# Kernel optimization log

Measured on AMD Instinct MI355X. Metric: run time of the kernel, lower is better.

## Reference

```python
import jax, jax.numpy as jnp
import numpy as np
import math

B, S, D, H = 2, 2048, 1024, 16
DK = D // H

def setup_inputs() -> dict:
    key = jax.random.key(0)
    ks = jax.random.split(key, 12)
    def xavier(k, shape):
        fan_in, fan_out = shape[1], shape[0]
        limit = math.sqrt(6.0 / (fan_in + fan_out))
        return jax.random.uniform(k, shape, jnp.float32, -limit, limit)
    inp = {
        'query': jax.random.normal(ks[0], (B, S, D), jnp.float32),
        'key':   jax.random.normal(ks[1], (B, S, D), jnp.float32),
        'value': jax.random.normal(ks[2], (B, S, D), jnp.float32),
        # causal mask, broadcast over heads: (B, 1, S, S), 1 = keep, 0 = mask
        'mask':  jnp.broadcast_to(jnp.tril(jnp.ones((S, S), jnp.int32)), (B, 1, S, S)),
        'Wq': xavier(ks[3], (D, D)), 'bq': jnp.zeros((D,), jnp.float32),
        'Wk': xavier(ks[4], (D, D)), 'bk': jnp.zeros((D,), jnp.float32),
        'Wv': xavier(ks[5], (D, D)), 'bv': jnp.zeros((D,), jnp.float32),
        'Wo': xavier(ks[6], (D, D)), 'bo': jnp.zeros((D,), jnp.float32),
    }
    return inp

def _split_heads(x):
    # (B, S, D) -> (B, H, S, DK)
    b, s, _ = x.shape
    return x.reshape(b, s, H, DK).transpose(0, 2, 1, 3)

def reference(query, key, value, mask, Wq, bq, Wk, bk, Wv, bv, Wo, bo):
    # torch nn.Linear: y = x @ W.T + b
    Q = _split_heads(query @ Wq.T + bq)   # (B,H,S,DK)
    K = _split_heads(key   @ Wk.T + bk)
    V = _split_heads(value @ Wv.T + bv)
    scores = jnp.einsum('bhqd,bhkd->bhqk', Q, K) / math.sqrt(DK)  # (B,H,S,S)
    scores = jnp.where(mask == 0, jnp.float32(-1e9), scores)
    attn = jax.nn.softmax(scores, axis=-1)  # dropout p=0 -> identity
    out = jnp.einsum('bhqk,bhkd->bhqd', attn, V)  # (B,H,S,DK)
    out = out.transpose(0, 2, 1, 3).reshape(query.shape[0], query.shape[1], D)
    return out @ Wo.T + bo
```

## Files before the change

### kernel.cpp

```cpp
#include <hip/hip_runtime.h>
#include <hip/hip_bf16.h>
#include <type_traits>


typedef __attribute__((ext_vector_type(8))) short short8;
typedef __attribute__((ext_vector_type(4))) short s16x4;
typedef __attribute__((ext_vector_type(4))) float floatx4;

__device__ __forceinline__ short f2bf(float x) {
    union { float f; unsigned u; } v; v.f = x;
    unsigned r = v.u + 0x7fffu + ((v.u >> 16) & 1u);
    return (short)(r >> 16);
}

__device__ __forceinline__ unsigned pk2bf(float a, float b) {
    union { __hip_bfloat162 h2; unsigned u; } cv;
    cv.h2 = __float22bfloat162_rn(make_float2(a, b));
    return cv.u;
}

__device__ __forceinline__ float fast_exp2(float x) {
#if __has_builtin(__builtin_amdgcn_exp2f)
    return __builtin_amdgcn_exp2f(x);
#else
    return __expf(x * 0.69314718056f);
#endif
}

typedef __attribute__((address_space(3))) short lds_short;
typedef __attribute__((address_space(1))) const short glb_short;
__device__ __forceinline__ void load_lds16(const void* g, void* l) {
    __builtin_amdgcn_global_load_lds((glb_short*)g, (lds_short*)l, 16, 0, 0);
}

__global__ __launch_bounds__(256) void cvt_all(
        const float* __restrict__ q, const float* __restrict__ k,
        const float* __restrict__ v,
        const float* __restrict__ wq, const float* __restrict__ wk,
        const float* __restrict__ wv, const float* __restrict__ wo,
        unsigned short* __restrict__ xq, unsigned short* __restrict__ xk,
        unsigned short* __restrict__ xv,
        unsigned short* __restrict__ wqb, unsigned short* __restrict__ wkb,
        unsigned short* __restrict__ wvb, unsigned short* __restrict__ wob) {
    const float* s; unsigned short* d;
    int bx = blockIdx.x;
    switch (blockIdx.y) {
        case 0: s = q; d = xq; break;
        case 1: s = k; d = xk; break;
        case 2: s = v; d = xv; break;
        default: {
            int wsel = bx >> 9; bx &= 511;
            s = (wsel == 0) ? wq : (wsel == 1) ? wk : (wsel == 2) ? wv : wo;
            d = (wsel == 0) ? wqb : (wsel == 1) ? wkb : (wsel == 2) ? wvb : wob;
        }
    }
    size_t i = ((size_t)bx * 256 + threadIdx.x) * 8;
    floatx4 a = *(const floatx4*)(s + i), b2 = *(const floatx4*)(s + i + 4);
    union { unsigned u[4]; short8 v8; } o;
    o.u[0] = pk2bf(a[0], a[1]);  o.u[1] = pk2bf(a[2], a[3]);
    o.u[2] = pk2bf(b2[0], b2[1]); o.u[3] = pk2bf(b2[2], b2[3]);
    *(short8*)(d + i) = o.v8;
}

__global__ __launch_bounds__(256) void gemm_qkv(
        const unsigned short* __restrict__ Xq, const unsigned short* __restrict__ Xk,
        const unsigned short* __restrict__ Xv,
        const unsigned short* __restrict__ Wq, const unsigned short* __restrict__ Wk,
        const unsigned short* __restrict__ Wv,
        const float* __restrict__ bq, const float* __restrict__ bk,
        const float* __restrict__ bv,
        unsigned short* __restrict__ Qb, unsigned short* __restrict__ Kb,
        unsigned short* __restrict__ Vb) {
    constexpr int K = 1024, N = 1024;
    __shared__ short As[128 * 64];
    __shared__ short Bs[128 * 64];
    const int t = threadIdx.x;
    const int slot = blockIdx.x;
    const int p = (slot & 7) + 8 * (slot >> 6);
    const int nx = (slot >> 3) & 7;
    const int chunk = p >> 5, my = p & 31;
    const unsigned short* A = chunk == 0 ? Xq : chunk == 1 ? Xk : Xv;
    const unsigned short* W = chunk == 0 ? Wq : chunk == 1 ? Wk : Wv;
    const float* bias        = chunk == 0 ? bq : chunk == 1 ? bk : bv;
    unsigned short* Y        = chunk == 0 ? Qb : chunk == 1 ? Kb : Vb;
    const float scale = chunk == 0 ? 0.1803368801f : 1.0f;
    const int m0 = my * 128, n0 = nx * 128;
    const int lane = t & 63, w = t >> 6;
    const int l16 = lane & 15, quad = lane >> 4;
    const int wm = w >> 1, wn = w & 1;
    const int srow8 = t >> 3, scs8 = t & 7;
    floatx4 acc[4][4] = {};

    for (int k0 = 0; k0 < K; k0 += 64) {
        __syncthreads();
        for (int i = 0; i < 4; i++) {
            const int row = i * 32 + srow8;
            const int cg = scs8 ^ (row & 7);
            load_lds16(A + (size_t)(m0 + row) * K + k0 + cg * 8, &As[i * 2048 + t * 8]);
            load_lds16(W + (size_t)(n0 + row) * K + k0 + cg * 8, &Bs[i * 2048 + t * 8]);
        }
        __syncthreads();

        for (int kc = 0; kc < 2; kc++) {
            short8 af[4], bf[4];
            for (int ms = 0; ms < 4; ms++) {
                const int row = wm * 64 + ms * 16 + l16;
                af[ms] = *(short8*)&As[row * 64 + (((kc << 2) | quad) ^ (row & 7)) * 8];
            }
            for (int ns = 0; ns < 4; ns++) {
                const int row = wn * 64 + ns * 16 + l16;
                bf[ns] = *(short8*)&Bs[row * 64 + (((kc << 2) | quad) ^ (row & 7)) * 8];
            }
            for (int ms = 0; ms < 4; ms++)
                for (int ns = 0; ns < 4; ns++)
                    acc[ms][ns] = __builtin_amdgcn_mfma_f32_16x16x32_bf16(
                            af[ms], bf[ns], acc[ms][ns], 0, 0, 0);
        }
    }

    for (int ms = 0; ms < 4; ms++)
        for (int ns = 0; ns < 4; ns++) {
            int col = n0 + wn * 64 + ns * 16 + l16;
            float bb = bias[col];
            for (int r = 0; r < 4; r++) {
                int row = m0 + wm * 64 + ms * 16 + quad * 4 + r;
                Y[(size_t)row * N + col] =
                    (unsigned short)f2bf((acc[ms][ns][r] + bb) * scale);
            }
        }
}

__global__ __launch_bounds__(256) void gemm_o(
        const unsigned short* __restrict__ A, const unsigned short* __restrict__ W,
        const float* __restrict__ bo, float* __restrict__ out) {
    constexpr int K = 1024, N = 1024;
    __shared__ short As[128 * 64];
    __shared__ short Bs[64 * 64];
    const int t = threadIdx.x;
    const int slot = blockIdx.x;
    const int z = slot >> 6;
    const int pm = (slot & 7) + 8 * (z >> 1);
    const int nx = ((slot >> 3) & 7) + 8 * (z & 1);
    const int m0 = pm * 128, n0 = nx * 64;
    const int lane = t & 63, w = t >> 6;
    const int l16 = lane & 15, quad = lane >> 4;
    const int wm = w >> 1, wn = w & 1;
    const int srow8 = t >> 3, scs8 = t & 7;
    floatx4 acc[4][2] = {};

    for (int k0 = 0; k0 < K; k0 += 64) {
        __syncthreads();
        for (int i = 0; i < 4; i++) {
            const int row = i * 32 + srow8;
            const int cg = scs8 ^ (row & 7);
            load_lds16(A + (size_t)(m0 + row) * K + k0 + cg * 8, &As[i * 2048 + t * 8]);
        }
        for (int i = 0; i < 2; i++) {
            const int row = i * 32 + srow8;
            const int cg = scs8 ^ (row & 7);
            load_lds16(W + (size_t)(n0 + row) * K + k0 + cg * 8, &Bs[i * 2048 + t * 8]);
        }
        __syncthreads();

        for (int kc = 0; kc < 2; kc++) {
            short8 af[4], bf[2];
            for (int ms = 0; ms < 4; ms++) {
                const int row = wm * 64 + ms * 16 + l16;
                af[ms] = *(short8*)&As[row * 64 + (((kc << 2) | quad) ^ (row & 7)) * 8];
            }
            for (int ns = 0; ns < 2; ns++) {
                const int row = wn * 32 + ns * 16 + l16;
                bf[ns] = *(short8*)&Bs[row * 64 + (((kc << 2) | quad) ^ (row & 7)) * 8];
            }
            for (int ms = 0; ms < 4; ms++)
                for (int ns = 0; ns < 2; ns++)
                    acc[ms][ns] = __builtin_amdgcn_mfma_f32_16x16x32_bf16(
                            af[ms], bf[ns], acc[ms][ns], 0, 0, 0);
        }
    }

    for (int ms = 0; ms < 4; ms++)
        for (int ns = 0; ns < 2; ns++) {
            int col = n0 + wn * 32 + ns * 16 + l16;
            float bb = bo[col];
            for (int r = 0; r < 4; r++) {
                int row = m0 + wm * 64 + ms * 16 + quad * 4 + r;
                out[(size_t)row * N + col] = acc[ms][ns][r] + bb;
            }
        }
}

__global__ __launch_bounds__(256) void attn_kernel(
        const unsigned short* __restrict__ Q, const unsigned short* __restrict__ Kp,
        const unsigned short* __restrict__ Vp, unsigned short* __restrict__ O) {
    __shared__ short Ks[64 * 72];
    __shared__ short Vt[64 * 72];
    __shared__ short Ps[4][16 * 72];
    const int t = threadIdx.x;
    const int bx = blockIdx.x;
    const int g = bx >> 8, c = bx & 255;
    const int dlt = c >> 5, bh = c & 31;
    const int unit = (g == 0) ? 31 - dlt : (g == 1) ? 23 - dlt
                   : (g == 2) ? 8 + dlt  : dlt;
    const int h = bh & 15, b = bh >> 4;
    const int q0 = unit * 64;
    const int lane = t & 63, w = t >> 6, l16 = lane & 15, quad = lane >> 4;
    const int krow = t >> 2, kcg = (t & 3) * 16;
    const int vp2 = t & 31, vg = t >> 5;

    short8 qf[2];
    {
        const size_t base = ((size_t)(b * 2048 + q0 + w * 16 + l16)) * 1024 + h * 64;
        qf[0] = *(const short8*)(Q + base + quad * 8);
        qf[1] = *(const short8*)(Q + base + 32 + quad * 8);
    }
    float l = 0.f;
    floatx4 o[4] = {};

    short8 ka, kb, va, vc;
    {
        const size_t kbse = ((size_t)(b * 2048 + krow)) * 1024 + h * 64 + kcg;
        ka = *(const short8*)(Kp + kbse);
        kb = *(const short8*)(Kp + kbse + 8);
        const size_t vbse = ((size_t)(b * 2048 + 2 * vp2)) * 1024 + h * 64 + vg * 8;
        va = *(const short8*)(Vp + vbse);
        vc = *(const short8*)(Vp + vbse + 1024);
    }

    for (int kv0 = 0; kv0 <= q0; kv0 += 64) {
        __syncthreads();
        *(short8*)&Ks[krow * 72 + kcg] = ka;
        *(short8*)&Ks[krow * 72 + kcg + 8] = kb;
        for (int i = 0; i < 8; i++) {
            unsigned pk = (unsigned)(unsigned short)va[i] |
                          ((unsigned)(unsigned short)vc[i] << 16);
            *(unsigned*)&Vt[(vg * 8 + i) * 72 + 2 * vp2] = pk;
        }
        __syncthreads();

        if (kv0 < q0) {
            const size_t kbse = ((size_t)(b * 2048 + kv0 + 64 + krow)) * 1024 + h * 64 + kcg;
            ka = *(const short8*)(Kp + kbse);
            kb = *(const short8*)(Kp + kbse + 8);
            const size_t vbse = ((size_t)(b * 2048 + kv0 + 64 + 2 * vp2)) * 1024 + h * 64 + vg * 8;
            va = *(const short8*)(Vp + vbse);
            vc = *(const short8*)(Vp + vbse + 1024);
        }

        floatx4 sv[4] = {};
        for (int hh = 0; hh < 4; hh++)
            for (int kc = 0; kc < 2; kc++) {
                short8 kf = *(short8*)&Ks[(hh * 16 + l16) * 72 + kc * 32 + quad * 8];
                sv[hh] = __builtin_amdgcn_mfma_f32_16x16x32_bf16(kf, qf[kc], sv[hh], 0, 0, 0);
            }

        {
            const bool needmask = (kv0 + 63 > q0 + w * 16);
            const int qg = q0 + w * 16 + l16;
            float ls = 0.f;
            for (int hh = 0; hh < 4; hh++) {
                float pv[4];
                for (int r = 0; r < 4; r++) {
                    int kv = kv0 + hh * 16 + quad * 4 + r;
                    float e = fast_exp2(sv[hh][r]);
                    pv[r] = (needmask && kv > qg) ? 0.f : e;
                    ls += pv[r];
                }
                union { unsigned u[2]; s16x4 v4; } pw;
                pw.u[0] = pk2bf(pv[0], pv[1]); pw.u[1] = pk2bf(pv[2], pv[3]);
                *(s16x4*)&Ps[w][l16 * 72 + hh * 16 + quad * 4] = pw.v4;
            }
            ls += __shfl_xor(ls, 16);
            ls += __shfl_xor(ls, 32);
            l += ls;
        }

        short8 p0 = *(short8*)&Ps[w][l16 * 72 + quad * 8];
        short8 p1 = *(short8*)&Ps[w][l16 * 72 + 32 + quad * 8];
        for (int nc = 0; nc < 4; nc++) {
            short8 vf0 = *(short8*)&Vt[(nc * 16 + l16) * 72 + quad * 8];
            short8 vf1 = *(short8*)&Vt[(nc * 16 + l16) * 72 + 32 + quad * 8];
            o[nc] = __builtin_amdgcn_mfma_f32_16x16x32_bf16(vf0, p0, o[nc], 0, 0, 0);
            o[nc] = __builtin_amdgcn_mfma_f32_16x16x32_bf16(vf1, p1, o[nc], 0, 0, 0);
        }
    }

    const float rl = 1.f / l;
    const size_t orow = ((size_t)(b * 2048 + q0 + w * 16 + l16)) * 1024 + h * 64;
    for (int nc = 0; nc < 4; nc++) {
        union { unsigned u[2]; s16x4 v4; } ow;
        ow.u[0] = pk2bf(o[nc][0] * rl, o[nc][1] * rl);
        ow.u[1] = pk2bf(o[nc][2] * rl, o[nc][3] * rl);
        *(s16x4*)(O + orow + nc * 16 + quad * 4) = ow.v4;
    }
}

extern "C" void kernel_launch(void* const* d_in, const int* in_sizes, int n_in,
                              void* d_out, int out_size, void* d_ws, size_t ws_size,
                              hipStream_t stream) {
    const float* query = (const float*)d_in[0];
    const float* key   = (const float*)d_in[1];
    const float* value = (const float*)d_in[2];
    const float* Wq = (const float*)d_in[4];
    const float* bq = (const float*)d_in[5];
    const float* Wk = (const float*)d_in[6];
    const float* bk = (const float*)d_in[7];
    const float* Wv = (const float*)d_in[8];
    const float* bv = (const float*)d_in[9];
    const float* Wo = (const float*)d_in[10];
    const float* bo = (const float*)d_in[11];

    const size_t NE = (size_t)4096 * 1024;
    const size_t WE = (size_t)1024 * 1024;
    unsigned short* Xq  = (unsigned short*)d_ws;
    unsigned short* Xk  = Xq + NE;
    unsigned short* Xv  = Xk + NE;
    unsigned short* Qb  = Xv + NE;
    unsigned short* Kb  = Qb + NE;
    unsigned short* Vb  = Kb + NE;
    unsigned short* Ob  = Vb + NE;
    unsigned short* Wqb = Ob + NE;
    unsigned short* Wkb = Wqb + WE;
    unsigned short* Wvb = Wkb + WE;
    unsigned short* Wob = Wvb + WE;

    cvt_all<<<dim3(2048, 4), 256, 0, stream>>>(query, key, value, Wq, Wk, Wv, Wo,
                                               Xq, Xk, Xv, Wqb, Wkb, Wvb, Wob);
    gemm_qkv<<<dim3(768), 256, 0, stream>>>(Xq, Xk, Xv, Wqb, Wkb, Wvb,
                                            bq, bk, bv, Qb, Kb, Vb);
    attn_kernel<<<dim3(1024), 256, 0, stream>>>(Qb, Kb, Vb, Ob);
    gemm_o<<<dim3(512), 256, 0, stream>>>(Ob, Wob, bo, (float*)d_out);
}
```

Measured before the change: 233.3 us.

## Fuse fp32-to-bf16 activation conversion into QKV GEMM and prioritize attention MFMAs

Drops the separate conversion pass over query/key/value. The QKV GEMM now reads fp32 activations straight into registers, converts them to bf16 and writes them to LDS, prefetching the next K-tile into registers while the current tile is computed. This removes the write and re-read of three bf16 activation copies, at the cost of extra registers and VALU conversion work inside the GEMM. Separately, it raises wave priority around the MFMA sections in the attention kernel so the matrix work is scheduled ahead of other waves.

```diff
diff --git a/kernel.cpp b/kernel.cpp
--- a/kernel.cpp
+++ b/kernel.cpp
@@ -33,27 +33,16 @@
     __builtin_amdgcn_global_load_lds((glb_short*)g, (lds_short*)l, 16, 0, 0);
 }
 
-__global__ __launch_bounds__(256) void cvt_all(
-        const float* __restrict__ q, const float* __restrict__ k,
-        const float* __restrict__ v,
+__global__ __launch_bounds__(256) void cvt_w(
         const float* __restrict__ wq, const float* __restrict__ wk,
         const float* __restrict__ wv, const float* __restrict__ wo,
-        unsigned short* __restrict__ xq, unsigned short* __restrict__ xk,
-        unsigned short* __restrict__ xv,
         unsigned short* __restrict__ wqb, unsigned short* __restrict__ wkb,
         unsigned short* __restrict__ wvb, unsigned short* __restrict__ wob) {
-    const float* s; unsigned short* d;
     int bx = blockIdx.x;
-    switch (blockIdx.y) {
-        case 0: s = q; d = xq; break;
-        case 1: s = k; d = xk; break;
-        case 2: s = v; d = xv; break;
-        default: {
-            int wsel = bx >> 9; bx &= 511;
-            s = (wsel == 0) ? wq : (wsel == 1) ? wk : (wsel == 2) ? wv : wo;
-            d = (wsel == 0) ? wqb : (wsel == 1) ? wkb : (wsel == 2) ? wvb : wob;
-        }
-    }
+    const int wsel = bx >> 9; bx &= 511;
+    const float* s = (wsel == 0) ? wq : (wsel == 1) ? wk : (wsel == 2) ? wv : wo;
+    unsigned short* d = (wsel == 0) ? wqb : (wsel == 1) ? wkb
+                      : (wsel == 2) ? wvb : wob;
     size_t i = ((size_t)bx * 256 + threadIdx.x) * 8;
     floatx4 a = *(const floatx4*)(s + i), b2 = *(const floatx4*)(s + i + 4);
     union { unsigned u[4]; short8 v8; } o;
@@ -63,8 +52,8 @@
 }
 
 __global__ __launch_bounds__(256) void gemm_qkv(
-        const unsigned short* __restrict__ Xq, const unsigned short* __restrict__ Xk,
-        const unsigned short* __restrict__ Xv,
+        const float* __restrict__ Xq, const float* __restrict__ Xk,
+        const float* __restrict__ Xv,
         const unsigned short* __restrict__ Wq, const unsigned short* __restrict__ Wk,
         const unsigned short* __restrict__ Wv,
         const float* __restrict__ bq, const float* __restrict__ bk,
@@ -79,10 +68,10 @@
     const int p = (slot & 7) + 8 * (slot >> 6);
     const int nx = (slot >> 3) & 7;
     const int chunk = p >> 5, my = p & 31;
-    const unsigned short* A = chunk == 0 ? Xq : chunk == 1 ? Xk : Xv;
+    const float* A          = chunk == 0 ? Xq : chunk == 1 ? Xk : Xv;
     const unsigned short* W = chunk == 0 ? Wq : chunk == 1 ? Wk : Wv;
-    const float* bias        = chunk == 0 ? bq : chunk == 1 ? bk : bv;
-    unsigned short* Y        = chunk == 0 ? Qb : chunk == 1 ? Kb : Vb;
+    const float* bias       = chunk == 0 ? bq : chunk == 1 ? bk : bv;
+    unsigned short* Y       = chunk == 0 ? Qb : chunk == 1 ? Kb : Vb;
     const float scale = chunk == 0 ? 0.1803368801f : 1.0f;
     const int m0 = my * 128, n0 = nx * 128;
     const int lane = t & 63, w = t >> 6;
@@ -90,16 +79,43 @@
     const int wm = w >> 1, wn = w & 1;
     const int srow8 = t >> 3, scs8 = t & 7;
     floatx4 acc[4][4] = {};
+    floatx4 ar[8];
+
+#pragma unroll
+    for (int i = 0; i < 4; i++) {
+        const int row = i * 32 + srow8;
+        const int cg = scs8 ^ (row & 7);
+        const float* pa = A + (size_t)(m0 + row) * K + cg * 8;
+        ar[2 * i]     = *(const floatx4*)pa;
+        ar[2 * i + 1] = *(const floatx4*)(pa + 4);
+    }
 
     for (int k0 = 0; k0 < K; k0 += 64) {
         __syncthreads();
+#pragma unroll
         for (int i = 0; i < 4; i++) {
+            union { unsigned u[4]; short8 v8; } oa;
+            oa.u[0] = pk2bf(ar[2 * i][0], ar[2 * i][1]);
+            oa.u[1] = pk2bf(ar[2 * i][2], ar[2 * i][3]);
+            oa.u[2] = pk2bf(ar[2 * i + 1][0], ar[2 * i + 1][1]);
+            oa.u[3] = pk2bf(ar[2 * i + 1][2], ar[2 * i + 1][3]);
+            *(short8*)&As[i * 2048 + t * 8] = oa.v8;
             const int row = i * 32 + srow8;
             const int cg = scs8 ^ (row & 7);
-            load_lds16(A + (size_t)(m0 + row) * K + k0 + cg * 8, &As[i * 2048 + t * 8]);
             load_lds16(W + (size_t)(n0 + row) * K + k0 + cg * 8, &Bs[i * 2048 + t * 8]);
         }
         __syncthreads();
+
+        if (k0 + 64 < K) {
+#pragma unroll
+            for (int i = 0; i < 4; i++) {
+                const int row = i * 32 + srow8;
+                const int cg = scs8 ^ (row & 7);
+                const float* pa = A + (size_t)(m0 + row) * K + k0 + 64 + cg * 8;
+                ar[2 * i]     = *(const floatx4*)pa;
+                ar[2 * i + 1] = *(const floatx4*)(pa + 4);
+            }
+        }
 
         for (int kc = 0; kc < 2; kc++) {
             short8 af[4], bf[4];
@@ -248,11 +264,13 @@
         }
 
         floatx4 sv[4] = {};
+        __builtin_amdgcn_s_setprio(1);
         for (int hh = 0; hh < 4; hh++)
             for (int kc = 0; kc < 2; kc++) {
                 short8 kf = *(short8*)&Ks[(hh * 16 + l16) * 72 + kc * 32 + quad * 8];
                 sv[hh] = __builtin_amdgcn_mfma_f32_16x16x32_bf16(kf, qf[kc], sv[hh], 0, 0, 0);
             }
+        __builtin_amdgcn_s_setprio(0);
 
         {
             const bool needmask = (kv0 + 63 > q0 + w * 16);
@@ -277,12 +295,14 @@
 
         short8 p0 = *(short8*)&Ps[w][l16 * 72 + quad * 8];
         short8 p1 = *(short8*)&Ps[w][l16 * 72 + 32 + quad * 8];
+        __builtin_amdgcn_s_setprio(1);
         for (int nc = 0; nc < 4; nc++) {
             short8 vf0 = *(short8*)&Vt[(nc * 16 + l16) * 72 + quad * 8];
             short8 vf1 = *(short8*)&Vt[(nc * 16 + l16) * 72 + 32 + quad * 8];
             o[nc] = __builtin_amdgcn_mfma_f32_16x16x32_bf16(vf0, p0, o[nc], 0, 0, 0);
             o[nc] = __builtin_amdgcn_mfma_f32_16x16x32_bf16(vf1, p1, o[nc], 0, 0, 0);
         }
+        __builtin_amdgcn_s_setprio(0);
     }
 
     const float rl = 1.f / l;
@@ -312,10 +332,7 @@
 
     const size_t NE = (size_t)4096 * 1024;
     const size_t WE = (size_t)1024 * 1024;
-    unsigned short* Xq  = (unsigned short*)d_ws;
-    unsigned short* Xk  = Xq + NE;
-    unsigned short* Xv  = Xk + NE;
-    unsigned short* Qb  = Xv + NE;
+    unsigned short* Qb  = (unsigned short*)d_ws;
     unsigned short* Kb  = Qb + NE;
     unsigned short* Vb  = Kb + NE;
     unsigned short* Ob  = Vb + NE;
@@ -324,9 +341,8 @@
     unsigned short* Wvb = Wkb + WE;
     unsigned short* Wob = Wvb + WE;
 
-    cvt_all<<<dim3(2048, 4), 256, 0, stream>>>(query, key, value, Wq, Wk, Wv, Wo,
-                                               Xq, Xk, Xv, Wqb, Wkb, Wvb, Wob);
-    gemm_qkv<<<dim3(768), 256, 0, stream>>>(Xq, Xk, Xv, Wqb, Wkb, Wvb,
+    cvt_w<<<dim3(2048), 256, 0, stream>>>(Wq, Wk, Wv, Wo, Wqb, Wkb, Wvb, Wob);
+    gemm_qkv<<<dim3(768), 256, 0, stream>>>(query, key, value, Wqb, Wkb, Wvb,
                                             bq, bk, bv, Qb, Kb, Vb);
     attn_kernel<<<dim3(1024), 256, 0, stream>>>(Qb, Kb, Vb, Ob);
     gemm_o<<<dim3(512), 256, 0, stream>>>(Ob, Wob, bo, (float*)d_out);
```

Measured after the change: 244.7 us. 4.9% more time.

## Double query tile per attention block to reuse K/V tiles across two row groups

Applied to the files above, without the earlier changes.

Each attention block now handles 128 query rows instead of 64, with each wave computing two 16-row groups that share the same K and V tiles in shared memory. This halves the grid to 512 blocks and halves the global K/V loads and LDS staging per query row. It also remaps the block-to-tile schedule for causal load balance and raises wave priority around the MFMA sections. The cost is higher register use from doubled accumulators, fewer blocks to fill the GPU, and extra masked work on the diagonal tiles.

```diff
diff --git a/kernel.cpp b/kernel.cpp
--- a/kernel.cpp
+++ b/kernel.cpp
@@ -195,27 +195,28 @@
         const unsigned short* __restrict__ Vp, unsigned short* __restrict__ O) {
     __shared__ short Ks[64 * 72];
     __shared__ short Vt[64 * 72];
-    __shared__ short Ps[4][16 * 72];
+    __shared__ short Ps[8][16 * 72];
     const int t = threadIdx.x;
     const int bx = blockIdx.x;
-    const int g = bx >> 8, c = bx & 255;
-    const int dlt = c >> 5, bh = c & 31;
-    const int unit = (g == 0) ? 31 - dlt : (g == 1) ? 23 - dlt
-                   : (g == 2) ? 8 + dlt  : dlt;
+    const int g = (bx >> 5) & 15, bh = bx & 31;
+    const int tile = (bx < 256) ? (15 - g) : (g - 8);
     const int h = bh & 15, b = bh >> 4;
-    const int q0 = unit * 64;
+    const int q0 = tile * 128;
     const int lane = t & 63, w = t >> 6, l16 = lane & 15, quad = lane >> 4;
     const int krow = t >> 2, kcg = (t & 3) * 16;
     const int vp2 = t & 31, vg = t >> 5;
 
-    short8 qf[2];
+    short8 qa[2], qb[2];
     {
-        const size_t base = ((size_t)(b * 2048 + q0 + w * 16 + l16)) * 1024 + h * 64;
-        qf[0] = *(const short8*)(Q + base + quad * 8);
-        qf[1] = *(const short8*)(Q + base + 32 + quad * 8);
-    }
-    float l = 0.f;
-    floatx4 o[4] = {};
+        const size_t baseA = ((size_t)(b * 2048 + q0 + w * 32 + l16)) * 1024 + h * 64;
+        qa[0] = *(const short8*)(Q + baseA + quad * 8);
+        qa[1] = *(const short8*)(Q + baseA + 32 + quad * 8);
+        const size_t baseB = baseA + (size_t)16 * 1024;
+        qb[0] = *(const short8*)(Q + baseB + quad * 8);
+        qb[1] = *(const short8*)(Q + baseB + 32 + quad * 8);
+    }
+    float lA = 0.f, lB = 0.f;
+    floatx4 oA[4] = {}, oB[4] = {};
 
     short8 ka, kb, va, vc;
     {
@@ -227,7 +228,8 @@
         vc = *(const short8*)(Vp + vbse + 1024);
     }
 
-    for (int kv0 = 0; kv0 <= q0; kv0 += 64) {
+    const int kv_hi = q0 + 128;
+    for (int kv0 = 0; kv0 < kv_hi; kv0 += 64) {
         __syncthreads();
         *(short8*)&Ks[krow * 72 + kcg] = ka;
         *(short8*)&Ks[krow * 72 + kcg + 8] = kb;
@@ -238,7 +240,7 @@
         }
         __syncthreads();
 
-        if (kv0 < q0) {
+        if (kv0 + 64 < kv_hi) {
             const size_t kbse = ((size_t)(b * 2048 + kv0 + 64 + krow)) * 1024 + h * 64 + kcg;
             ka = *(const short8*)(Kp + kbse);
             kb = *(const short8*)(Kp + kbse + 8);
@@ -247,51 +249,92 @@
             vc = *(const short8*)(Vp + vbse + 1024);
         }
 
-        floatx4 sv[4] = {};
+        floatx4 sA[4] = {}, sB[4] = {};
+        __builtin_amdgcn_s_setprio(1);
         for (int hh = 0; hh < 4; hh++)
             for (int kc = 0; kc < 2; kc++) {
                 short8 kf = *(short8*)&Ks[(hh * 16 + l16) * 72 + kc * 32 + quad * 8];
-                sv[hh] = __builtin_amdgcn_mfma_f32_16x16x32_bf16(kf, qf[kc], sv[hh], 0, 0, 0);
-            }
+                sA[hh] = __builtin_amdgcn_mfma_f32_16x16x32_bf16(kf, qa[kc], sA[hh], 0, 0, 0);
+                sB[hh] = __builtin_amdgcn_mfma_f32_16x16x32_bf16(kf, qb[kc], sB[hh], 0, 0, 0);
+            }
+        __builtin_amdgcn_s_setprio(0);
 
         {
-            const bool needmask = (kv0 + 63 > q0 + w * 16);
-            const int qg = q0 + w * 16 + l16;
+            const bool nm = (kv0 + 63 > q0 + w * 32);
+            const int qg = q0 + w * 32 + l16;
             float ls = 0.f;
             for (int hh = 0; hh < 4; hh++) {
                 float pv[4];
                 for (int r = 0; r < 4; r++) {
                     int kv = kv0 + hh * 16 + quad * 4 + r;
-                    float e = fast_exp2(sv[hh][r]);
-                    pv[r] = (needmask && kv > qg) ? 0.f : e;
+                    float e = fast_exp2(sA[hh][r]);
+                    pv[r] = (nm && kv > qg) ? 0.f : e;
                     ls += pv[r];
                 }
                 union { unsigned u[2]; s16x4 v4; } pw;
                 pw.u[0] = pk2bf(pv[0], pv[1]); pw.u[1] = pk2bf(pv[2], pv[3]);
-                *(s16x4*)&Ps[w][l16 * 72 + hh * 16 + quad * 4] = pw.v4;
+                *(s16x4*)&Ps[2 * w][l16 * 72 + hh * 16 + quad * 4] = pw.v4;
             }
             ls += __shfl_xor(ls, 16);
             ls += __shfl_xor(ls, 32);
-            l += ls;
-        }
-
-        short8 p0 = *(short8*)&Ps[w][l16 * 72 + quad * 8];
-        short8 p1 = *(short8*)&Ps[w][l16 * 72 + 32 + quad * 8];
+            lA += ls;
+        }
+        {
+            const bool nm = (kv0 + 63 > q0 + w * 32 + 16);
+            const int qg = q0 + w * 32 + 16 + l16;
+            float ls = 0.f;
+            for (int hh = 0; hh < 4; hh++) {
+                float pv[4];
+                for (int r = 0; r < 4; r++) {
+                    int kv = kv0 + hh * 16 + quad * 4 + r;
+                    float e = fast_exp2(sB[hh][r]);
+                    pv[r] = (nm && kv > qg) ? 0.f : e;
+                    ls += pv[r];
+                }
+                union { unsigned u[2]; s16x4 v4; } pw;
+                pw.u[0] = pk2bf(pv[0], pv[1]); pw.u[1] = pk2bf(pv[2], pv[3]);
+                *(s16x4*)&Ps[2 * w + 1][l16 * 72 + hh * 16 + quad * 4] = pw.v4;
+            }
+            ls += __shfl_xor(ls, 16);
+            ls += __shfl_xor(ls, 32);
+            lB += ls;
+        }
+
+        short8 pa0 = *(short8*)&Ps[2 * w][l16 * 72 + quad * 8];
+        short8 pa1 = *(short8*)&Ps[2 * w][l16 * 72 + 32 + quad * 8];
+        short8 pb0 = *(short8*)&Ps[2 * w + 1][l16 * 72 + quad * 8];
+        short8 pb1 = *(short8*)&Ps[2 * w + 1][l16 * 72 + 32 + quad * 8];
+        __builtin_amdgcn_s_setprio(1);
         for (int nc = 0; nc < 4; nc++) {
             short8 vf0 = *(short8*)&Vt[(nc * 16 + l16) * 72 + quad * 8];
             short8 vf1 = *(short8*)&Vt[(nc * 16 + l16) * 72 + 32 + quad * 8];
-            o[nc] = __builtin_amdgcn_mfma_f32_16x16x32_bf16(vf0, p0, o[nc], 0, 0, 0);
-            o[nc] = __builtin_amdgcn_mfma_f32_16x16x32_bf16(vf1, p1, o[nc], 0, 0, 0);
-        }
-    }
-
-    const float rl = 1.f / l;
-    const size_t orow = ((size_t)(b * 2048 + q0 + w * 16 + l16)) * 1024 + h * 64;
-    for (int nc = 0; nc < 4; nc++) {
-        union { unsigned u[2]; s16x4 v4; } ow;
-        ow.u[0] = pk2bf(o[nc][0] * rl, o[nc][1] * rl);
-        ow.u[1] = pk2bf(o[nc][2] * rl, o[nc][3] * rl);
-        *(s16x4*)(O + orow + nc * 16 + quad * 4) = ow.v4;
+            oA[nc] = __builtin_amdgcn_mfma_f32_16x16x32_bf16(vf0, pa0, oA[nc], 0, 0, 0);
+            oA[nc] = __builtin_amdgcn_mfma_f32_16x16x32_bf16(vf1, pa1, oA[nc], 0, 0, 0);
+            oB[nc] = __builtin_amdgcn_mfma_f32_16x16x32_bf16(vf0, pb0, oB[nc], 0, 0, 0);
+            oB[nc] = __builtin_amdgcn_mfma_f32_16x16x32_bf16(vf1, pb1, oB[nc], 0, 0, 0);
+        }
+        __builtin_amdgcn_s_setprio(0);
+    }
+
+    {
+        const float rl = 1.f / lA;
+        const size_t orow = ((size_t)(b * 2048 + q0 + w * 32 + l16)) * 1024 + h * 64;
+        for (int nc = 0; nc < 4; nc++) {
+            union { unsigned u[2]; s16x4 v4; } ow;
+            ow.u[0] = pk2bf(oA[nc][0] * rl, oA[nc][1] * rl);
+            ow.u[1] = pk2bf(oA[nc][2] * rl, oA[nc][3] * rl);
+            *(s16x4*)(O + orow + nc * 16 + quad * 4) = ow.v4;
+        }
+    }
+    {
+        const float rl = 1.f / lB;
+        const size_t orow = ((size_t)(b * 2048 + q0 + w * 32 + 16 + l16)) * 1024 + h * 64;
+        for (int nc = 0; nc < 4; nc++) {
+            union { unsigned u[2]; s16x4 v4; } ow;
+            ow.u[0] = pk2bf(oB[nc][0] * rl, oB[nc][1] * rl);
+            ow.u[1] = pk2bf(oB[nc][2] * rl, oB[nc][3] * rl);
+            *(s16x4*)(O + orow + nc * 16 + quad * 4) = ow.v4;
+        }
     }
 }
 
@@ -328,6 +371,6 @@
                                                Xq, Xk, Xv, Wqb, Wkb, Wvb, Wob);
     gemm_qkv<<<dim3(768), 256, 0, stream>>>(Xq, Xk, Xv, Wqb, Wkb, Wvb,
                                             bq, bk, bv, Qb, Kb, Vb);
-    attn_kernel<<<dim3(1024), 256, 0, stream>>>(Qb, Kb, Vb, Ob);
+    attn_kernel<<<dim3(512), 256, 0, stream>>>(Qb, Kb, Vb, Ob);
     gemm_o<<<dim3(512), 256, 0, stream>>>(Ob, Wob, bo, (float*)d_out);
 }
```

Result: slower. 245.4 us (+5.2%).
